# Performance work log

Measured on AMD Instinct MI355X. Metric: run time of the kernel, lower is better.

## Reference

```python
import jax, jax.numpy as jnp
import numpy as np

B, T, H_IMG, HID, ACT = 128, 100, 72, 512, 2


def _conv(x, w, b, stride, pad):
    y = jax.lax.conv_general_dilated(
        x, w, (stride, stride), [(pad, pad), (pad, pad)],
        dimension_numbers=('NCHW', 'OIHW', 'NCHW'))
    return y + b[None, :, None, None]


def _encode(images, cw1, cb1, cw2, cb2, cw3, cb3, fw1, fb1, fw2, fb2, fw3, fb3):
    relu = jax.nn.relu
    x = relu(_conv(images, cw1, cb1, 3, 2))   # [B,64,24,24]
    x = relu(_conv(x, cw2, cb2, 3, 2))        # [B,64,9,9]
    x = relu(_conv(x, cw3, cb3, 3, 2))        # [B,64,4,4]
    x = x.reshape(x.shape[0], -1)             # [B,1024]
    x = relu(x @ fw1.T + fb1)
    x = relu(x @ fw2.T + fb2)
    return x @ fw3.T + fb3                    # [B,512]


def _gru(actions, h0, w_ih, w_hh, b_ih, b_hh):
    # precompute input projections for all steps: [T,B,3H]
    gi = jnp.einsum('btd,gd->tbg', actions, w_ih) + b_ih

    def step(h, gi_t):
        gh = h @ w_hh.T + b_hh
        i_r, i_i, i_n = jnp.split(gi_t, 3, axis=-1)
        h_r, h_i, h_n = jnp.split(gh, 3, axis=-1)
        r = jax.nn.sigmoid(i_r + h_r)
        z = jax.nn.sigmoid(i_i + h_i)
        n = jnp.tanh(i_n + r * h_n)
        hy = n + z * (h - n)
        return hy, hy

    hT, outs = jax.lax.scan(step, h0, gi)
    return jnp.transpose(outs, (1, 0, 2)), hT  # batch_first output


def setup_inputs() -> dict:
    key = jax.random.key(0)
    ks = jax.random.split(key, 16)
    s = 0.05
    return {
        'images': jax.random.normal(ks[0], (B, 3, H_IMG, H_IMG), jnp.float32),
        'actions': jax.random.normal(ks[1], (B, T, ACT), jnp.float32),
        'cw1': jax.random.normal(ks[2], (64, 3, 5, 5), jnp.float32) * s,
        'cb1': jax.random.normal(ks[3], (64,), jnp.float32) * s,
        'cw2': jax.random.normal(ks[4], (64, 64, 3, 3), jnp.float32) * s,
        'cb2': jax.random.normal(ks[5], (64,), jnp.float32) * s,
        'cw3': jax.random.normal(ks[6], (64, 64, 3, 3), jnp.float32) * s,
        'cb3': jax.random.normal(ks[7], (64,), jnp.float32) * s,
        'fw1': jax.random.normal(ks[8], (1024, 1024), jnp.float32) * 0.02,
        'fb1': jax.random.normal(ks[9], (1024,), jnp.float32) * 0.02,
        'fw2': jax.random.normal(ks[10], (512, 1024), jnp.float32) * 0.02,
        'fb2': jax.random.normal(ks[11], (512,), jnp.float32) * 0.02,
        'fw3': jax.random.normal(ks[12], (512, 512), jnp.float32) * 0.02,
        'fb3': jax.random.normal(ks[13], (512,), jnp.float32) * 0.02,
        'w_ih': jax.random.normal(ks[14], (3 * HID, ACT), jnp.float32) * 0.05,
        'w_hh': jax.random.normal(ks[15], (3 * HID, HID), jnp.float32) * 0.04,
        'b_ih': jnp.zeros((3 * HID,), jnp.float32),
        'b_hh': jnp.zeros((3 * HID,), jnp.float32),
    }


def reference(images, actions, cw1, cb1, cw2, cb2, cw3, cb3,
              fw1, fb1, fw2, fb2, fw3, fb3, w_ih, w_hh, b_ih, b_hh):
    # Encode the start image to a 512-d representation (BigBasicConv),
    # then integrate the action sequence with the hand-rolled GRU,
    # initial hidden state = start representation.
    h0 = _encode(images, cw1, cb1, cw2, cb2, cw3, cb3,
                 fw1, fb1, fw2, fb2, fw3, fb3)
    output, hT = _gru(actions, h0, w_ih, w_hh, b_ih, b_hh)
    return output, hT
```

## Files before the change

### kernel.cpp

```cpp
#include <hip/hip_runtime.h>
#include <cstdint>

#define BB   128
#define TT   100
#define HID  512

typedef __attribute__((ext_vector_type(4))) float f32x4;
typedef __attribute__((ext_vector_type(8))) short short8;
typedef __attribute__((ext_vector_type(4))) short short4_t;

__device__ __forceinline__ short f2bf(float x) {
  unsigned u = __float_as_uint(x);
  unsigned r = (u + 0x7fffu + ((u >> 16) & 1u)) >> 16;
  return (short)r;
}
__device__ __forceinline__ float bf2f(short s) {
  return __uint_as_float(((unsigned)(unsigned short)s) << 16);
}


__global__ __launch_bounds__(384) void conv1_k(const float* __restrict__ in,
                                               const float* __restrict__ w,
                                               const float* __restrict__ bias,
                                               float* __restrict__ out) {
  const int b = blockIdx.x / 24, oy = blockIdx.x % 24;
  __shared__ __attribute__((aligned(16))) float in_s[3][5][76];
  __shared__ __attribute__((aligned(16))) float ws[64][76];
  const int tid = threadIdx.x;
  for (int i = tid; i < 3 * 5 * 76; i += 384) {
    int ic = i / 380, rem = i % 380, r = rem / 76, p = rem % 76;
    int iy = oy * 3 + r - 2, ix = p - 2;
    in_s[ic][r][p] = (iy >= 0 && iy < 72 && ix >= 0 && ix < 72)
                       ? in[((long)(b * 3 + ic) * 72 + iy) * 72 + ix] : 0.f;
  }
  for (int i = tid; i < 64 * 75; i += 384) ws[i / 75][i % 75] = w[i];
  __syncthreads();

  const int ox = tid % 24;
  const int og = tid / 24;
  float patch[75];
  #pragma unroll
  for (int ic = 0; ic < 3; ic++)
    #pragma unroll
    for (int ky = 0; ky < 5; ky++)
      #pragma unroll
      for (int kx = 0; kx < 5; kx++)
        patch[(ic * 5 + ky) * 5 + kx] = in_s[ic][ky][ox * 3 + kx];

  #pragma unroll
  for (int j = 0; j < 4; j++) {
    int oc = og + 16 * j;
    float s = bias[oc];
    const float* wrow = ws[oc];
    #pragma unroll
    for (int k4 = 0; k4 < 18; k4++) {
      f32x4 wq = *(const f32x4*)(wrow + 4 * k4);
      s += patch[4 * k4 + 0] * wq[0];
      s += patch[4 * k4 + 1] * wq[1];
      s += patch[4 * k4 + 2] * wq[2];
      s += patch[4 * k4 + 3] * wq[3];
    }
    s += patch[72] * wrow[72];
    s += patch[73] * wrow[73];
    s += patch[74] * wrow[74];
    out[((long)(b * 64 + oc) * 24 + oy) * 24 + ox] = fmaxf(s, 0.f);
  }
}

template <int IC, int IH, int IW, int OC, int OH, int OW>
__global__ void convs3(const float* __restrict__ in, const float* __restrict__ w,
                       const float* __restrict__ bias, float* __restrict__ out) {
  const int b = blockIdx.x / OH, oy = blockIdx.x % OH;
  constexpr int PW = 3 * OW;
  constexpr int NT = (OC / 2) * OW;
  __shared__ __attribute__((aligned(16))) float in_s[8][3][PW];
  __shared__ __attribute__((aligned(16))) float w_s[OC][100];
  const int tid = threadIdx.x;
  const int oc = tid / OW, ox = tid % OW;
  float s0 = bias[oc], s1 = bias[oc + OC / 2];
  for (int cc = 0; cc < IC; cc += 8) {
    __syncthreads();
    for (int i = tid; i < 8 * 3 * PW; i += NT) {
      int ic = i / (3 * PW), r = (i / PW) % 3, p = i % PW;
      int iy = oy * 3 - 2 + r, ix = p - 2;
      in_s[ic][r][p] = (iy >= 0 && iy < IH && ix >= 0 && ix < IW)
                         ? in[((long)(b * IC + cc + ic) * IH + iy) * IW + ix] : 0.f;
    }
    for (int i = tid; i < OC * 8 * 9; i += NT) {
      int o = i / 72, r = i % 72;
      w_s[o][(r / 9) * 12 + (r % 9)] = w[(long)(o * IC + cc + r / 9) * 9 + r % 9];
    }
    __syncthreads();
    #pragma unroll
    for (int ic = 0; ic < 8; ic++) {
      const float* wr0 = &w_s[oc][ic * 12];
      const float* wr1 = &w_s[oc + OC / 2][ic * 12];
      f32x4 wa = *(const f32x4*)wr0, wb = *(const f32x4*)(wr0 + 4);
      f32x4 va = *(const f32x4*)wr1, vb = *(const f32x4*)(wr1 + 4);
      float wA[9] = {wa[0], wa[1], wa[2], wa[3], wb[0], wb[1], wb[2], wb[3], wr0[8]};
      float wB[9] = {va[0], va[1], va[2], va[3], vb[0], vb[1], vb[2], vb[3], wr1[8]};
      #pragma unroll
      for (int ky = 0; ky < 3; ky++)
        #pragma unroll
        for (int kx = 0; kx < 3; kx++) {
          float iv = in_s[ic][ky][ox * 3 + kx];
          s0 += iv * wA[ky * 3 + kx];
          s1 += iv * wB[ky * 3 + kx];
        }
    }
  }
  out[((long)(b * OC + oc) * OH + oy) * OW + ox] = fmaxf(s0, 0.f);
  out[((long)(b * OC + oc + OC / 2) * OH + oy) * OW + ox] = fmaxf(s1, 0.f);
}

template <int K, int N, bool RELU>
__global__ __launch_bounds__(256) void fc_k(const float* __restrict__ A,
                                            const float* __restrict__ W,
                                            const float* __restrict__ bias,
                                            float* __restrict__ C) {
  const int nb = N / 64;
  const int rb = (blockIdx.x / nb) * 16, cb = (blockIdx.x % nb) * 64;
  __shared__ __attribute__((aligned(16))) float As[16][68];
  __shared__ __attribute__((aligned(16))) float Ws[64][68];
  const int tid = threadIdx.x;
  const int c = tid & 63, rg = tid >> 6;
  float acc[4] = {0.f, 0.f, 0.f, 0.f};
  for (int kc = 0; kc < K; kc += 64) {
    for (int i = tid; i < 16 * 64; i += 256)
      As[i >> 6][i & 63] = A[(long)(rb + (i >> 6)) * K + kc + (i & 63)];
    for (int i = tid; i < 64 * 64; i += 256)
      Ws[i >> 6][i & 63] = W[(long)(cb + (i >> 6)) * K + kc + (i & 63)];
    __syncthreads();
    #pragma unroll
    for (int k4 = 0; k4 < 16; k4++) {
      f32x4 wq = *(const f32x4*)&Ws[c][4 * k4];
      f32x4 a0 = *(const f32x4*)&As[rg][4 * k4];
      f32x4 a1 = *(const f32x4*)&As[rg + 4][4 * k4];
      f32x4 a2 = *(const f32x4*)&As[rg + 8][4 * k4];
      f32x4 a3 = *(const f32x4*)&As[rg + 12][4 * k4];
      #pragma unroll
      for (int kk = 0; kk < 4; kk++) {
        acc[0] += a0[kk] * wq[kk];
        acc[1] += a1[kk] * wq[kk];
        acc[2] += a2[kk] * wq[kk];
        acc[3] += a3[kk] * wq[kk];
      }
    }
    __syncthreads();
  }
  float bv = bias[cb + c];
  #pragma unroll
  for (int i = 0; i < 4; i++) {
    float v = acc[i] + bv;
    if (RELU) v = fmaxf(v, 0.f);
    C[(long)(rb + rg + 4 * i) * N + cb + c] = v;
  }
}

__global__ __launch_bounds__(192, 1) void gru_k(
    const float* __restrict__ actions, const float* __restrict__ w_ih,
    const float* __restrict__ w_hh, const float* __restrict__ b_ih,
    const float* __restrict__ b_hh, const float* __restrict__ h0,
    float* __restrict__ out, float* __restrict__ hT, unsigned* __restrict__ bar) {
  const int bg = blockIdx.x >> 5;
  const int hg = blockIdx.x & 31;
  const int tid = threadIdx.x;
  const int wv = tid >> 6;
  const int lane = tid & 63;
  const int n16 = lane & 15;
  const int quad = lane >> 4;

  __shared__ short h_hi[16][520];
  __shared__ short h_lo[16][520];
  __shared__ float act_s[16][2 * TT];
  __shared__ float gh_s[3][16][17];
  __shared__ float bih_s[48], bhh_s[48], wih0_s[48], wih1_s[48];

  short8 whi[16], wlo[16];
  {
    const int grow = wv * HID + hg * 16 + n16;
    const float* wr = w_hh + (long)grow * HID + quad * 8;
    #pragma unroll
    for (int ks = 0; ks < 16; ks++) {
      f32x4 v0 = *(const f32x4*)(wr + ks * 32);
      f32x4 v1 = *(const f32x4*)(wr + ks * 32 + 4);
      short8 hi, lo;
      #pragma unroll
      for (int j = 0; j < 4; j++) {
        short h1 = f2bf(v0[j]); hi[j] = h1;     lo[j] = f2bf(v0[j] - bf2f(h1));
        short h2 = f2bf(v1[j]); hi[j + 4] = h2; lo[j + 4] = f2bf(v1[j] - bf2f(h2));
      }
      whi[ks] = hi; wlo[ks] = lo;
    }
  }
  for (int i = tid; i < 48; i += 192) {
    int row = (i >> 4) * HID + hg * 16 + (i & 15);
    bih_s[i] = b_ih[row];
    bhh_s[i] = b_hh[row];
    wih0_s[i] = w_ih[row * 2];
    wih1_s[i] = w_ih[row * 2 + 1];
  }
  for (int i = tid; i < 16 * 2 * TT; i += 192) {
    int m = i / (2 * TT), r = i % (2 * TT);
    act_s[m][r] = actions[(long)(bg * 16 + m) * (2 * TT) + r];
  }
  for (int i = tid; i < 2048; i += 192) {
    int m = i >> 7, k4 = (i & 127) << 2;
    f32x4 v = *(const f32x4*)(h0 + (long)(bg * 16 + m) * HID + k4);
    short4_t sh, sl;
    #pragma unroll
    for (int c2 = 0; c2 < 4; c2++) {
      short hh = f2bf(v[c2]); sh[c2] = hh; sl[c2] = f2bf(v[c2] - bf2f(hh));
    }
    *(short4_t*)&h_hi[m][k4] = sh;
    *(short4_t*)&h_lo[m][k4] = sl;
  }
  __syncthreads();

  unsigned* my_bar = bar + bg * 32;

  #pragma unroll 1
  for (int t = 0; t < TT; t++) {
    f32x4 a0 = {0.f, 0.f, 0.f, 0.f}, a1 = a0, a2 = a0;
    #pragma unroll
    for (int ks = 0; ks < 16; ks++) {
      short8 ah = *(const short8*)&h_hi[n16][ks * 32 + quad * 8];
      short8 al = *(const short8*)&h_lo[n16][ks * 32 + quad * 8];
      a0 = __builtin_amdgcn_mfma_f32_16x16x32_bf16(ah, whi[ks], a0, 0, 0, 0);
      a1 = __builtin_amdgcn_mfma_f32_16x16x32_bf16(al, whi[ks], a1, 0, 0, 0);
      a2 = __builtin_amdgcn_mfma_f32_16x16x32_bf16(ah, wlo[ks], a2, 0, 0, 0);
    }
    #pragma unroll
    for (int r = 0; r < 4; r++)
      gh_s[wv][quad * 4 + r][n16] = a0[r] + a1[r] + a2[r];
    __syncthreads();

    if (tid < 128) {
      const int m = tid >> 3;
      const int n0 = (tid & 7) << 1;
      const float x0 = act_s[m][2 * t], x1 = act_s[m][2 * t + 1];
      float hy[2];
      #pragma unroll
      for (int q = 0; q < 2; q++) {
        int n = n0 + q;
        float hr = gh_s[0][m][n] + bhh_s[n];
        float hz = gh_s[1][m][n] + bhh_s[16 + n];
        float hn = gh_s[2][m][n] + bhh_s[32 + n];
        float ir = x0 * wih0_s[n]      + x1 * wih1_s[n]      + bih_s[n];
        float iz = x0 * wih0_s[16 + n] + x1 * wih1_s[16 + n] + bih_s[16 + n];
        float in_ = x0 * wih0_s[32 + n] + x1 * wih1_s[32 + n] + bih_s[32 + n];
        float rg = 1.f / (1.f + __expf(-(ir + hr)));
        float zg = 1.f / (1.f + __expf(-(iz + hz)));
        float nx = in_ + rg * hn;
        float ng = 1.f - 2.f / (__expf(2.f * nx) + 1.f);
        float hprev = bf2f(h_hi[m][hg * 16 + n]) + bf2f(h_lo[m][hg * 16 + n]);
        hy[q] = ng + zg * (hprev - ng);
      }
      unsigned long long pack = (unsigned long long)__float_as_uint(hy[0]) |
                                ((unsigned long long)__float_as_uint(hy[1]) << 32);
      __hip_atomic_store(
          (unsigned long long*)&out[((long)(bg * 16 + m) * TT + t) * HID + hg * 16 + n0],
          pack, __ATOMIC_RELAXED, __HIP_MEMORY_SCOPE_AGENT);
      if (t == TT - 1)
        *(unsigned long long*)&hT[(long)(bg * 16 + m) * HID + hg * 16 + n0] = pack;
    }
    __syncthreads();

    if (t < TT - 1) {
      if (tid == 0) {
        const unsigned target = 32u * (unsigned)(t + 1);
        unsigned prev = __hip_atomic_fetch_add(my_bar, 1u, __ATOMIC_RELAXED,
                                               __HIP_MEMORY_SCOPE_AGENT);
        if (prev + 1u < target) {
          while (__hip_atomic_load(my_bar, __ATOMIC_RELAXED,
                                   __HIP_MEMORY_SCOPE_AGENT) < target)
            __builtin_amdgcn_s_sleep(1);
        }
      }
      __syncthreads();
      unsigned long long vbuf[22];
      #pragma unroll
      for (int u = 0; u < 21; u++) {
        int i = tid + u * 192;
        int m = i >> 8, j = (i & 255) << 1;
        vbuf[u] = __hip_atomic_load(
            (const unsigned long long*)(out + ((long)(bg * 16 + m) * TT + t) * HID + j),
            __ATOMIC_RELAXED, __HIP_MEMORY_SCOPE_AGENT);
      }
      if (tid < 64) {
        int i = 4032 + tid;
        int m = i >> 8, j = (i & 255) << 1;
        vbuf[21] = __hip_atomic_load(
            (const unsigned long long*)(out + ((long)(bg * 16 + m) * TT + t) * HID + j),
            __ATOMIC_RELAXED, __HIP_MEMORY_SCOPE_AGENT);
      }
      #pragma unroll
      for (int u = 0; u < 21; u++) {
        int i = tid + u * 192;
        int m = i >> 8, j = (i & 255) << 1;
        unsigned long long v = vbuf[u];
        float f0 = __uint_as_float((unsigned)v);
        float f1 = __uint_as_float((unsigned)(v >> 32));
        short s0 = f2bf(f0);
        h_hi[m][j] = s0; h_lo[m][j] = f2bf(f0 - bf2f(s0));
        short s1 = f2bf(f1);
        h_hi[m][j + 1] = s1; h_lo[m][j + 1] = f2bf(f1 - bf2f(s1));
      }
      if (tid < 64) {
        int i = 4032 + tid;
        int m = i >> 8, j = (i & 255) << 1;
        unsigned long long v = vbuf[21];
        float f0 = __uint_as_float((unsigned)v);
        float f1 = __uint_as_float((unsigned)(v >> 32));
        short s0 = f2bf(f0);
        h_hi[m][j] = s0; h_lo[m][j] = f2bf(f0 - bf2f(s0));
        short s1 = f2bf(f1);
        h_hi[m][j + 1] = s1; h_lo[m][j + 1] = f2bf(f1 - bf2f(s1));
      }
      __syncthreads();
    }
  }
}

extern "C" void kernel_launch(void* const* d_in, const int* in_sizes, int n_in,
                              void* d_out, int out_size, void* d_ws, size_t ws_size,
                              hipStream_t stream) {
  const float* images  = (const float*)d_in[0];
  const float* actions = (const float*)d_in[1];
  const float* cw1 = (const float*)d_in[2];
  const float* cb1 = (const float*)d_in[3];
  const float* cw2 = (const float*)d_in[4];
  const float* cb2 = (const float*)d_in[5];
  const float* cw3 = (const float*)d_in[6];
  const float* cb3 = (const float*)d_in[7];
  const float* fw1 = (const float*)d_in[8];
  const float* fb1 = (const float*)d_in[9];
  const float* fw2 = (const float*)d_in[10];
  const float* fb2 = (const float*)d_in[11];
  const float* fw3 = (const float*)d_in[12];
  const float* fb3 = (const float*)d_in[13];
  const float* w_ih = (const float*)d_in[14];
  const float* w_hh = (const float*)d_in[15];
  const float* b_ih = (const float*)d_in[16];
  const float* b_hh = (const float*)d_in[17];

  char* ws = (char*)d_ws;
  unsigned* bar = (unsigned*)ws;
  float* a1 = (float*)(ws + 1024);
  float* a2 = a1 + (long)128 * 64 * 576;
  float* a3 = a2 + (long)128 * 64 * 81;
  float* f1 = a3 + (long)128 * 1024;
  float* f2 = f1 + (long)128 * 1024;
  float* h0 = f2 + (long)128 * 512;

  float* out = (float*)d_out;
  float* hT  = out + (long)BB * TT * HID;

  hipMemsetAsync(bar, 0, 1024, stream);
  conv1_k<<<128 * 24, 384, 0, stream>>>(images, cw1, cb1, a1);
  convs3<64, 24, 24, 64, 9, 9><<<128 * 9, 288, 0, stream>>>(a1, cw2, cb2, a2);
  convs3<64, 9, 9, 64, 4, 4><<<128 * 4, 128, 0, stream>>>(a2, cw3, cb3, a3);
  fc_k<1024, 1024, true><<<128, 256, 0, stream>>>(a3, fw1, fb1, f1);
  fc_k<1024, 512, true><<<64, 256, 0, stream>>>(f1, fw2, fb2, f2);
  fc_k<512, 512, false><<<64, 256, 0, stream>>>(f2, fw3, fb3, h0);
  gru_k<<<256, 192, 0, stream>>>(actions, w_ih, w_hh, b_ih, b_hh, h0, out, hT, bar);
}
```

Before: 717.4 us.

## Use split-bf16 MFMA for FC layers and two-output conv1 threads

```diff
diff --git a/kernel.cpp b/kernel.cpp
--- a/kernel.cpp
+++ b/kernel.cpp
@@ -6,6 +6,7 @@
 #define HID  512
 
 typedef __attribute__((ext_vector_type(4))) float f32x4;
+typedef __attribute__((ext_vector_type(2))) float f32x2;
 typedef __attribute__((ext_vector_type(8))) short short8;
 typedef __attribute__((ext_vector_type(4))) short short4_t;
 
@@ -18,8 +19,26 @@
   return __uint_as_float(((unsigned)(unsigned short)s) << 16);
 }
 
-
-__global__ __launch_bounds__(384) void conv1_k(const float* __restrict__ in,
+__global__ __launch_bounds__(256) void wsplit_k(const float* __restrict__ w,
+                                                unsigned short* __restrict__ hi,
+                                                unsigned short* __restrict__ lo,
+                                                int nq) {
+  int i = blockIdx.x * 256 + threadIdx.x;
+  const int stride = gridDim.x * 256;
+  for (; i < nq; i += stride) {
+    f32x4 v = *(const f32x4*)(w + 4 * (long)i);
+    short4_t h, l;
+    #pragma unroll
+    for (int c = 0; c < 4; c++) {
+      short hh = f2bf(v[c]); h[c] = hh; l[c] = f2bf(v[c] - bf2f(hh));
+    }
+    *(short4_t*)(hi + 4 * (long)i) = h;
+    *(short4_t*)(lo + 4 * (long)i) = l;
+  }
+}
+
+
+__global__ __launch_bounds__(192) void conv1_k(const float* __restrict__ in,
                                                const float* __restrict__ w,
                                                const float* __restrict__ bias,
                                                float* __restrict__ out) {
@@ -27,43 +46,52 @@
   __shared__ __attribute__((aligned(16))) float in_s[3][5][76];
   __shared__ __attribute__((aligned(16))) float ws[64][76];
   const int tid = threadIdx.x;
-  for (int i = tid; i < 3 * 5 * 76; i += 384) {
+  for (int i = tid; i < 3 * 5 * 76; i += 192) {
     int ic = i / 380, rem = i % 380, r = rem / 76, p = rem % 76;
     int iy = oy * 3 + r - 2, ix = p - 2;
     in_s[ic][r][p] = (iy >= 0 && iy < 72 && ix >= 0 && ix < 72)
                        ? in[((long)(b * 3 + ic) * 72 + iy) * 72 + ix] : 0.f;
   }
-  for (int i = tid; i < 64 * 75; i += 384) ws[i / 75][i % 75] = w[i];
+  for (int i = tid; i < 64 * 75; i += 192) ws[i / 75][i % 75] = w[i];
   __syncthreads();
 
-  const int ox = tid % 24;
-  const int og = tid / 24;
-  float patch[75];
+  const int ox2 = tid % 12;
+  const int og = tid / 12;
+  float strip[15][8];
   #pragma unroll
   for (int ic = 0; ic < 3; ic++)
     #pragma unroll
-    for (int ky = 0; ky < 5; ky++)
-      #pragma unroll
-      for (int kx = 0; kx < 5; kx++)
-        patch[(ic * 5 + ky) * 5 + kx] = in_s[ic][ky][ox * 3 + kx];
+    for (int ky = 0; ky < 5; ky++) {
+      const float* bp = &in_s[ic][ky][6 * ox2];
+      #pragma unroll
+      for (int h = 0; h < 4; h++) {
+        f32x2 u = *(const f32x2*)(bp + 2 * h);
+        strip[ic * 5 + ky][2 * h] = u[0];
+        strip[ic * 5 + ky][2 * h + 1] = u[1];
+      }
+    }
 
   #pragma unroll
   for (int j = 0; j < 4; j++) {
-    int oc = og + 16 * j;
-    float s = bias[oc];
+    const int oc = og + 16 * j;
+    float s0 = bias[oc], s1 = bias[oc];
     const float* wrow = ws[oc];
     #pragma unroll
     for (int k4 = 0; k4 < 18; k4++) {
       f32x4 wq = *(const f32x4*)(wrow + 4 * k4);
-      s += patch[4 * k4 + 0] * wq[0];
-      s += patch[4 * k4 + 1] * wq[1];
-      s += patch[4 * k4 + 2] * wq[2];
-      s += patch[4 * k4 + 3] * wq[3];
-    }
-    s += patch[72] * wrow[72];
-    s += patch[73] * wrow[73];
-    s += patch[74] * wrow[74];
-    out[((long)(b * 64 + oc) * 24 + oy) * 24 + ox] = fmaxf(s, 0.f);
+      #pragma unroll
+      for (int q = 0; q < 4; q++) {
+        const int k = 4 * k4 + q, i5 = k / 5, kx = k % 5;
+        s0 += strip[i5][kx] * wq[q];
+        s1 += strip[i5][kx + 3] * wq[q];
+      }
+    }
+    s0 += strip[14][2] * wrow[72]; s1 += strip[14][5] * wrow[72];
+    s0 += strip[14][3] * wrow[73]; s1 += strip[14][6] * wrow[73];
+    s0 += strip[14][4] * wrow[74]; s1 += strip[14][7] * wrow[74];
+    long o = ((long)(b * 64 + oc) * 24 + oy) * 24 + 2 * ox2;
+    out[o] = fmaxf(s0, 0.f);
+    out[o + 1] = fmaxf(s1, 0.f);
   }
 }
 
@@ -114,46 +142,59 @@
 }
 
 template <int K, int N, bool RELU>
-__global__ __launch_bounds__(256) void fc_k(const float* __restrict__ A,
-                                            const float* __restrict__ W,
-                                            const float* __restrict__ bias,
-                                            float* __restrict__ C) {
-  const int nb = N / 64;
-  const int rb = (blockIdx.x / nb) * 16, cb = (blockIdx.x % nb) * 64;
-  __shared__ __attribute__((aligned(16))) float As[16][68];
-  __shared__ __attribute__((aligned(16))) float Ws[64][68];
+__global__ __launch_bounds__(128) void fc_mfma(const float* __restrict__ A,
+                                               const unsigned short* __restrict__ wh,
+                                               const unsigned short* __restrict__ wl,
+                                               const float* __restrict__ bias,
+                                               float* __restrict__ C) {
+  const int nb = N / 32;
+  const int rb = (blockIdx.x / nb) * 16, cb = (blockIdx.x % nb) * 32;
+  __shared__ __attribute__((aligned(16))) short A_hi[16][K + 8];
+  __shared__ __attribute__((aligned(16))) short A_lo[16][K + 8];
   const int tid = threadIdx.x;
-  const int c = tid & 63, rg = tid >> 6;
-  float acc[4] = {0.f, 0.f, 0.f, 0.f};
-  for (int kc = 0; kc < K; kc += 64) {
-    for (int i = tid; i < 16 * 64; i += 256)
-      As[i >> 6][i & 63] = A[(long)(rb + (i >> 6)) * K + kc + (i & 63)];
-    for (int i = tid; i < 64 * 64; i += 256)
-      Ws[i >> 6][i & 63] = W[(long)(cb + (i >> 6)) * K + kc + (i & 63)];
-    __syncthreads();
-    #pragma unroll
-    for (int k4 = 0; k4 < 16; k4++) {
-      f32x4 wq = *(const f32x4*)&Ws[c][4 * k4];
-      f32x4 a0 = *(const f32x4*)&As[rg][4 * k4];
-      f32x4 a1 = *(const f32x4*)&As[rg + 4][4 * k4];
-      f32x4 a2 = *(const f32x4*)&As[rg + 8][4 * k4];
-      f32x4 a3 = *(const f32x4*)&As[rg + 12][4 * k4];
-      #pragma unroll
-      for (int kk = 0; kk < 4; kk++) {
-        acc[0] += a0[kk] * wq[kk];
-        acc[1] += a1[kk] * wq[kk];
-        acc[2] += a2[kk] * wq[kk];
-        acc[3] += a3[kk] * wq[kk];
-      }
-    }
-    __syncthreads();
-  }
-  float bv = bias[cb + c];
+  const int wv = tid >> 6, lane = tid & 63, n16 = lane & 15, quad = lane >> 4;
+
+  for (int i = tid; i < 16 * (K / 4); i += 128) {
+    int row = i / (K / 4), q = i % (K / 4);
+    f32x4 v = *(const f32x4*)(A + (long)(rb + row) * K + 4 * q);
+    short4_t sh, sl;
+    #pragma unroll
+    for (int c = 0; c < 4; c++) {
+      short hh = f2bf(v[c]); sh[c] = hh; sl[c] = f2bf(v[c] - bf2f(hh));
+    }
+    *(short4_t*)&A_hi[row][4 * q] = sh;
+    *(short4_t*)&A_lo[row][4 * q] = sl;
+  }
+  __syncthreads();
+
+  const int col = cb + wv * 16 + n16;
+  f32x4 a0 = {0.f, 0.f, 0.f, 0.f}, a1 = a0, a2 = a0;
+  constexpr int NP = K / 512;
+  #pragma unroll 1
+  for (int p = 0; p < NP; p++) {
+    short8 fh[16], fl[16];
+    const unsigned short* wb0 = wh + (long)col * K + p * 512 + quad * 8;
+    const unsigned short* wb1 = wl + (long)col * K + p * 512 + quad * 8;
+    #pragma unroll
+    for (int ks = 0; ks < 16; ks++) {
+      fh[ks] = *(const short8*)(wb0 + ks * 32);
+      fl[ks] = *(const short8*)(wb1 + ks * 32);
+    }
+    #pragma unroll
+    for (int ks = 0; ks < 16; ks++) {
+      short8 ah = *(const short8*)&A_hi[n16][p * 512 + ks * 32 + quad * 8];
+      short8 al = *(const short8*)&A_lo[n16][p * 512 + ks * 32 + quad * 8];
+      a0 = __builtin_amdgcn_mfma_f32_16x16x32_bf16(ah, fh[ks], a0, 0, 0, 0);
+      a1 = __builtin_amdgcn_mfma_f32_16x16x32_bf16(al, fh[ks], a1, 0, 0, 0);
+      a2 = __builtin_amdgcn_mfma_f32_16x16x32_bf16(ah, fl[ks], a2, 0, 0, 0);
+    }
+  }
+  const float bv = bias[col];
   #pragma unroll
-  for (int i = 0; i < 4; i++) {
-    float v = acc[i] + bv;
+  for (int r = 0; r < 4; r++) {
+    float v = a0[r] + a1[r] + a2[r] + bv;
     if (RELU) v = fmaxf(v, 0.f);
-    C[(long)(rb + rg + 4 * i) * N + cb + c] = v;
+    C[(long)(rb + quad * 4 + r) * N + col] = v;
   }
 }
 
@@ -352,16 +393,25 @@
   float* f1 = a3 + (long)128 * 1024;
   float* f2 = f1 + (long)128 * 1024;
   float* h0 = f2 + (long)128 * 512;
+  unsigned short* wfh1 = (unsigned short*)(h0 + 65536);
+  unsigned short* wfl1 = wfh1 + (long)1048576;
+  unsigned short* wfh2 = wfl1 + (long)1048576;
+  unsigned short* wfl2 = wfh2 + (long)524288;
+  unsigned short* wfh3 = wfl2 + (long)524288;
+  unsigned short* wfl3 = wfh3 + (long)262144;
 
   float* out = (float*)d_out;
   float* hT  = out + (long)BB * TT * HID;
 
   hipMemsetAsync(bar, 0, 1024, stream);
-  conv1_k<<<128 * 24, 384, 0, stream>>>(images, cw1, cb1, a1);
+  wsplit_k<<<256, 256, 0, stream>>>(fw1, wfh1, wfl1, 262144);
+  wsplit_k<<<128, 256, 0, stream>>>(fw2, wfh2, wfl2, 131072);
+  wsplit_k<<<64, 256, 0, stream>>>(fw3, wfh3, wfl3, 65536);
+  conv1_k<<<128 * 24, 192, 0, stream>>>(images, cw1, cb1, a1);
   convs3<64, 24, 24, 64, 9, 9><<<128 * 9, 288, 0, stream>>>(a1, cw2, cb2, a2);
   convs3<64, 9, 9, 64, 4, 4><<<128 * 4, 128, 0, stream>>>(a2, cw3, cb3, a3);
-  fc_k<1024, 1024, true><<<128, 256, 0, stream>>>(a3, fw1, fb1, f1);
-  fc_k<1024, 512, true><<<64, 256, 0, stream>>>(f1, fw2, fb2, f2);
-  fc_k<512, 512, false><<<64, 256, 0, stream>>>(f2, fw3, fb3, h0);
+  fc_mfma<1024, 1024, true><<<256, 128, 0, stream>>>(a3, wfh1, wfl1, fb1, f1);
+  fc_mfma<1024, 512, true><<<128, 128, 0, stream>>>(f1, wfh2, wfl2, fb2, f2);
+  fc_mfma<512, 512, false><<<128, 128, 0, stream>>>(f2, wfh3, wfl3, fb3, h0);
   gru_k<<<256, 192, 0, stream>>>(actions, w_ih, w_hh, b_ih, b_hh, h0, out, hT, bar);
 }
```

After: 645.1 us. 10.1% less time.
